# Kernel tuning notes

Hardware: AMD Instinct MI355X
Metric: run time of the kernel (lower is better)

## Reference

```python
import jax, jax.numpy as jnp
import numpy as np

EPS = 4.0 / 30.0  # epsilon / epoch from source
P_KEEP = 0.95     # random-response probability of keeping a column


def setup_inputs() -> dict:
    key = jax.random.key(0)
    ks = jax.random.split(key, 10)
    B, F, H, C = 262144, 160, 128, 10
    x1 = jax.random.normal(ks[0], (B, F), dtype=jnp.float32)
    x2 = jax.random.normal(ks[1], (B, F), dtype=jnp.float32)
    W1 = jax.random.normal(ks[2], (F, H), dtype=jnp.float32) * 0.05
    b1 = jax.random.normal(ks[3], (H,), dtype=jnp.float32) * 0.05
    W2 = jax.random.normal(ks[4], (F, H), dtype=jnp.float32) * 0.05
    b2 = jax.random.normal(ks[5], (H,), dtype=jnp.float32) * 0.05
    Ws = jax.random.normal(ks[6], (H, C), dtype=jnp.float32) * 0.05
    bs = jax.random.normal(ks[7], (C,), dtype=jnp.float32) * 0.05
    # standard Laplace(0,1) noise; scaled by sensitivity/eps inside reference
    noise_std = jax.random.laplace(ks[8], (B, H), dtype=jnp.float32)
    rr_uniform = jax.random.uniform(ks[9], (H,), dtype=jnp.float32)
    return {"x1": x1, "x2": x2, "W1": W1, "b1": b1, "W2": W2, "b2": b2,
            "Ws": Ws, "bs": bs, "noise_std": noise_std, "rr_uniform": rr_uniform}


def reference(x1, x2, W1, b1, W2, b2, Ws, bs, noise_std, rr_uniform):
    # client 1: linear -> DP noise -> random-response mask
    out1 = x1 @ W1 + b1                              # [B, 128]
    one_norm = jnp.sum(jnp.abs(out1), axis=1)        # per-row L1 norm
    sensitivity = jnp.max(one_norm) - jnp.min(one_norm)
    sensitivity = jax.lax.stop_gradient(sensitivity)  # .item() in torch: non-diff
    noise_mul = sensitivity / EPS
    out1 = out1 + noise_std * noise_mul              # Laplace(0, noise_mul) sample
    rr_mask = (rr_uniform < P_KEEP).astype(out1.dtype)  # [128] 0/1 mask
    out1 = out1 * rr_mask
    # client 2: plain linear
    out2 = x2 @ W2 + b2                              # [B, 128]
    # server: element-wise min then linear head
    server_input = jnp.minimum(out1, out2)
    return server_input @ Ws + bs                    # [B, 10]
```

## Files before the change

### kernel.cpp

```cpp
#include <hip/hip_runtime.h>
#include <hip/hip_bf16.h>
#include <float.h>


typedef __bf16 bf16x8 __attribute__((ext_vector_type(8)));
typedef __bf16 bf16x4 __attribute__((ext_vector_type(4)));
typedef float  f32x4  __attribute__((ext_vector_type(4)));

#define FDIM 160
#define HDIM 128
#define SROW 132

#define GL2LDS(g, l) __builtin_amdgcn_global_load_lds( \
    (const __attribute__((address_space(1))) unsigned int*)(g), \
    (__attribute__((address_space(3))) unsigned int*)(l), 16, 0, 0)

__global__ void k0_prep(const float* __restrict__ W1, const float* __restrict__ W2,
                        unsigned int* __restrict__ mmx,
                        __bf16* __restrict__ w1t, __bf16* __restrict__ w2t) {
    int tid = blockIdx.x * 256 + threadIdx.x;
    if (tid == 0) { mmx[0] = 0x7F7FFFFFu;  mmx[1] = 0u; }
    for (int idx = tid; idx < FDIM * HDIM; idx += gridDim.x * 256) {
        int k = idx >> 7, n = idx & 127;
        w1t[n * FDIM + k] = (__bf16)W1[idx];
        w2t[n * FDIM + k] = (__bf16)W2[idx];
    }
}

__device__ __forceinline__ bf16x8 pack8(f32x4 lo, f32x4 hi) {
    bf16x8 a;
    a[0] = (__bf16)lo[0]; a[1] = (__bf16)lo[1]; a[2] = (__bf16)lo[2]; a[3] = (__bf16)lo[3];
    a[4] = (__bf16)hi[0]; a[5] = (__bf16)hi[1]; a[6] = (__bf16)hi[2]; a[7] = (__bf16)hi[3];
    return a;
}

__global__ __launch_bounds__(256, 4) void k1_sens(
    const float* __restrict__ x1, const float* __restrict__ b1,
    const __bf16* __restrict__ w1t, unsigned int* __restrict__ mmx, int B)
{
    __shared__ __align__(16) char stg[2][10 * 1024];
    __shared__ float nbuf[2][4][16];

    const int lane = threadIdx.x & 63;
    const int wv   = threadIdx.x >> 6;
    const int m    = lane & 15;
    const int q    = lane >> 4;

    bf16x8 wf[2][5];
    f32x4  bv[2];
    #pragma unroll
    for (int cc = 0; cc < 2; ++cc) {
        const int ct = 2 * wv + cc;
        bv[cc] = *(const f32x4*)&b1[ct * 16 + q * 4];
        #pragma unroll
        for (int ks = 0; ks < 5; ++ks)
            wf[cc][ks] = *(const bf16x8*)(w1t + (ct * 16 + m) * FDIM + ks * 32 + q * 8);
    }

    const int nslab = B >> 4;
    auto stage = [&](int buf, int slab) {
        const float* rowp = x1 + (size_t)((slab << 4) + m) * FDIM + q * 8;
        for (int c = wv; c < 10; c += 4)
            GL2LDS(rowp + (c >> 1) * 32 + (c & 1) * 4, &stg[buf][c * 1024]);
    };

    float wmin = FLT_MAX, wmax = 0.0f;
    int it = blockIdx.x, cur = 0, iter = 0;
    stage(0, it);
    for (; it < nslab; it += gridDim.x) {
        asm volatile("s_waitcnt vmcnt(0)" ::: "memory");
        __syncthreads();
        if (iter > 0 && wv == 0 && lane < 16) {
            const int pb = (iter - 1) & 1;
            float nrm = nbuf[pb][0][m] + nbuf[pb][1][m] + nbuf[pb][2][m] + nbuf[pb][3][m];
            wmin = fminf(wmin, nrm); wmax = fmaxf(wmax, nrm);
        }
        if (it + (int)gridDim.x < nslab) stage(cur ^ 1, it + gridDim.x);

        f32x4 acc[2] = { bv[0], bv[1] };
        #pragma unroll
        for (int ks = 0; ks < 5; ++ks) {
            f32x4 lo = *(const f32x4*)&stg[cur][(2 * ks) * 1024 + lane * 16];
            f32x4 hi = *(const f32x4*)&stg[cur][(2 * ks + 1) * 1024 + lane * 16];
            bf16x8 a = pack8(lo, hi);
            acc[0] = __builtin_amdgcn_mfma_f32_16x16x32_bf16(wf[0][ks], a, acc[0], 0, 0, 0);
            acc[1] = __builtin_amdgcn_mfma_f32_16x16x32_bf16(wf[1][ks], a, acc[1], 0, 0, 0);
        }
        float part = 0.0f;
        #pragma unroll
        for (int cc = 0; cc < 2; ++cc)
            #pragma unroll
            for (int reg = 0; reg < 4; ++reg) part += fabsf(acc[cc][reg]);
        part += __shfl_xor(part, 16, 64);
        part += __shfl_xor(part, 32, 64);
        if (lane < 16) nbuf[iter & 1][wv][m] = part;
        cur ^= 1; ++iter;
    }
    __syncthreads();
    if (iter > 0 && wv == 0 && lane < 16) {
        const int pb = (iter - 1) & 1;
        float nrm = nbuf[pb][0][m] + nbuf[pb][1][m] + nbuf[pb][2][m] + nbuf[pb][3][m];
        wmin = fminf(wmin, nrm); wmax = fmaxf(wmax, nrm);
    }
    if (wv == 0) {
        #pragma unroll
        for (int off = 1; off < 16; off <<= 1) {
            wmin = fminf(wmin, __shfl_xor(wmin, off, 64));
            wmax = fmaxf(wmax, __shfl_xor(wmax, off, 64));
        }
        if (lane == 0) {
            atomicMin(&mmx[0], __float_as_uint(wmin));
            atomicMax(&mmx[1], __float_as_uint(wmax));
        }
    }
}

__global__ __launch_bounds__(256, 2) void k2_main(
    const float* __restrict__ x1, const float* __restrict__ x2,
    const float* __restrict__ b1, const float* __restrict__ b2,
    const float* __restrict__ Ws, const float* __restrict__ bs,
    const float* __restrict__ noise, const float* __restrict__ rru,
    const __bf16* __restrict__ w1t, const __bf16* __restrict__ w2t,
    const unsigned int* __restrict__ mmx, float* __restrict__ out, int B)
{
    __shared__ __align__(16) char   stg[2][28 * 1024];
    __shared__ __align__(16) __bf16 sbuf[16 * SROW];
    __shared__ __align__(16) float  obuf[160];

    const int lane = threadIdx.x & 63;
    const int wv   = threadIdx.x >> 6;
    const int m    = lane & 15;
    const int q    = lane >> 4;

    const float noise_mul = (__uint_as_float(mmx[1]) - __uint_as_float(mmx[0])) * 7.5f;

    bf16x8 wf1[2][5], wf2[2][5];
    f32x4  bv1[2], bv2[2];
    unsigned rmask = 0;
    #pragma unroll
    for (int cc = 0; cc < 2; ++cc) {
        const int ct = 2 * wv + cc;
        bv1[cc] = *(const f32x4*)&b1[ct * 16 + q * 4];
        bv2[cc] = *(const f32x4*)&b2[ct * 16 + q * 4];
        f32x4 r4 = *(const f32x4*)&rru[ct * 16 + q * 4];
        #pragma unroll
        for (int reg = 0; reg < 4; ++reg)
            if (r4[reg] < 0.95f) rmask |= 1u << (cc * 4 + reg);
        #pragma unroll
        for (int ks = 0; ks < 5; ++ks) {
            wf1[cc][ks] = *(const bf16x8*)(w1t + (ct * 16 + m) * FDIM + ks * 32 + q * 8);
            wf2[cc][ks] = *(const bf16x8*)(w2t + (ct * 16 + m) * FDIM + ks * 32 + q * 8);
        }
    }
    bf16x8 wsf[4];
    #pragma unroll
    for (int ks2 = 0; ks2 < 4; ++ks2)
        #pragma unroll
        for (int j = 0; j < 8; ++j) {
            int h = ks2 * 32 + q * 8 + j;
            wsf[ks2][j] = (__bf16)((m < 10) ? Ws[h * 10 + m] : 0.0f);
        }
    const float bsv = (m < 10) ? bs[m] : 0.0f;

    const int nslab = B >> 4;
    auto stage = [&](int buf, int slab) {
        const int r0 = slab << 4;
        const float* x1p = x1 + (size_t)(r0 + m) * FDIM + q * 8;
        const float* x2p = x2 + (size_t)(r0 + m) * FDIM + q * 8;
        const float* nzp = noise + (size_t)(r0 + m) * HDIM + q * 4;
        #pragma unroll
        for (int j = 0; j < 7; ++j) {
            const int c = wv * 7 + j;
            const float* g;
            if (c < 10)      g = x1p + (c >> 1) * 32 + (c & 1) * 4;
            else if (c < 20) g = x2p + ((c - 10) >> 1) * 32 + ((c - 10) & 1) * 4;
            else             g = nzp + (c - 20) * 16;
            GL2LDS(g, &stg[buf][c * 1024]);
        }
    };

    int it = blockIdx.x, cur = 0;
    stage(0, it);
    for (; it < nslab; it += gridDim.x) {
        asm volatile("s_waitcnt vmcnt(0)" ::: "memory");
        __syncthreads();
        if (it + (int)gridDim.x < nslab) stage(cur ^ 1, it + gridDim.x);

        f32x4 acc1[2] = { bv1[0], bv1[1] }, acc2[2] = { bv2[0], bv2[1] };
        #pragma unroll
        for (int ks = 0; ks < 5; ++ks) {
            f32x4 lo1 = *(const f32x4*)&stg[cur][(2 * ks) * 1024 + lane * 16];
            f32x4 hi1 = *(const f32x4*)&stg[cur][(2 * ks + 1) * 1024 + lane * 16];
            f32x4 lo2 = *(const f32x4*)&stg[cur][(10 + 2 * ks) * 1024 + lane * 16];
            f32x4 hi2 = *(const f32x4*)&stg[cur][(11 + 2 * ks) * 1024 + lane * 16];
            bf16x8 a1 = pack8(lo1, hi1), a2 = pack8(lo2, hi2);
            acc1[0] = __builtin_amdgcn_mfma_f32_16x16x32_bf16(wf1[0][ks], a1, acc1[0], 0, 0, 0);
            acc1[1] = __builtin_amdgcn_mfma_f32_16x16x32_bf16(wf1[1][ks], a1, acc1[1], 0, 0, 0);
            acc2[0] = __builtin_amdgcn_mfma_f32_16x16x32_bf16(wf2[0][ks], a2, acc2[0], 0, 0, 0);
            acc2[1] = __builtin_amdgcn_mfma_f32_16x16x32_bf16(wf2[1][ks], a2, acc2[1], 0, 0, 0);
        }
        #pragma unroll
        for (int cc = 0; cc < 2; ++cc) {
            f32x4 nz = *(const f32x4*)&stg[cur][(20 + 2 * wv + cc) * 1024 + lane * 16];
            bf16x4 pk;
            #pragma unroll
            for (int reg = 0; reg < 4; ++reg) {
                float v1 = acc1[cc][reg] + nz[reg] * noise_mul;
                v1 = ((rmask >> (cc * 4 + reg)) & 1u) ? v1 : 0.0f;
                pk[reg] = (__bf16)fminf(v1, acc2[cc][reg]);
            }
            *(bf16x4*)&sbuf[m * SROW + (2 * wv + cc) * 16 + q * 4] = pk;
        }
        __syncthreads();
        if (wv == 0) {
            f32x4 d = { bsv, bsv, bsv, bsv };
            #pragma unroll
            for (int ks2 = 0; ks2 < 4; ++ks2) {
                bf16x8 sf = *(const bf16x8*)&sbuf[m * SROW + ks2 * 32 + q * 8];
                d = __builtin_amdgcn_mfma_f32_16x16x32_bf16(sf, wsf[ks2], d, 0, 0, 0);
            }
            if (m < 10) {
                #pragma unroll
                for (int reg = 0; reg < 4; ++reg)
                    obuf[(q * 4 + reg) * 10 + m] = d[reg];
            }
            asm volatile("s_waitcnt lgkmcnt(0)" ::: "memory");
            if (lane < 40) {
                f32x4 o = *(const f32x4*)&obuf[lane * 4];
                *(f32x4*)(out + (size_t)it * 160 + lane * 4) = o;
            }
        }
        cur ^= 1;
    }
}

extern "C" void kernel_launch(void* const* d_in, const int* in_sizes, int n_in,
                              void* d_out, int out_size, void* d_ws, size_t ws_size,
                              hipStream_t stream) {
    const float* x1    = (const float*)d_in[0];
    const float* x2    = (const float*)d_in[1];
    const float* W1    = (const float*)d_in[2];
    const float* b1    = (const float*)d_in[3];
    const float* W2    = (const float*)d_in[4];
    const float* b2    = (const float*)d_in[5];
    const float* Ws    = (const float*)d_in[6];
    const float* bs    = (const float*)d_in[7];
    const float* noise = (const float*)d_in[8];
    const float* rru   = (const float*)d_in[9];
    float* out = (float*)d_out;
    const int B = in_sizes[0] / FDIM;

    unsigned int* mmx = (unsigned int*)d_ws;
    __bf16* w1t = (__bf16*)((char*)d_ws + 256);
    __bf16* w2t = (__bf16*)((char*)d_ws + 256 + 40960);

    hipLaunchKernelGGL(k0_prep, dim3(64), dim3(256), 0, stream, W1, W2, mmx, w1t, w2t);
    hipLaunchKernelGGL(k1_sens, dim3(1024), dim3(256), 0, stream, x1, b1, w1t, mmx, B);
    hipLaunchKernelGGL(k2_main, dim3(512), dim3(256), 0, stream,
                       x1, x2, b1, b2, Ws, bs, noise, rru, w1t, w2t, mmx, out, B);
}
```

Before: 481.2 us.

## Triple-buffer staging with partial vmcnt waits and register-prefetched noise

Both kernels move from double-buffered LDS staging with full vmcnt(0) waits to a three-stage ring with prefetch distance two, waiting only on the oldest batch through partial vmcnt counts and raw s_barrier. In the main kernel the noise tile no longer goes through LDS; it is loaded straight into registers one iteration ahead. The output head is now computed redundantly by every wave, and each wave writes one quarter of the rows directly to global memory, which removes the obuf round-trip. The aim is to keep more loads in flight and reduce barrier stalls. The cost is more LDS per block, hand-counted vmcnt values that must match the real number of outstanding loads, and redundant loads of slab 0 when a prefetch runs past the end.

```diff
diff --git a/kernel.cpp b/kernel.cpp
--- a/kernel.cpp
+++ b/kernel.cpp
@@ -38,7 +38,7 @@
     const float* __restrict__ x1, const float* __restrict__ b1,
     const __bf16* __restrict__ w1t, unsigned int* __restrict__ mmx, int B)
 {
-    __shared__ __align__(16) char stg[2][10 * 1024];
+    __shared__ __align__(16) char stg[3][10 * 1024];
     __shared__ float nbuf[2][4][16];
 
     const int lane = threadIdx.x & 63;
@@ -58,43 +58,60 @@
     }
 
     const int nslab = B >> 4;
+    const int G = gridDim.x;
+
     auto stage = [&](int buf, int slab) {
+        if (slab >= nslab) slab = 0;
         const float* rowp = x1 + (size_t)((slab << 4) + m) * FDIM + q * 8;
-        for (int c = wv; c < 10; c += 4)
-            GL2LDS(rowp + (c >> 1) * 32 + (c & 1) * 4, &stg[buf][c * 1024]);
+        if (wv < 2) {
+            #pragma unroll
+            for (int j = 0; j < 3; ++j) {
+                const int c = wv * 3 + j;
+                GL2LDS(rowp + (c >> 1) * 32 + (c & 1) * 4, &stg[buf][c * 1024]);
+            }
+        } else {
+            #pragma unroll
+            for (int j = 0; j < 2; ++j) {
+                const int c = 6 + (wv - 2) * 2 + j;
+                GL2LDS(rowp + (c >> 1) * 32 + (c & 1) * 4, &stg[buf][c * 1024]);
+            }
+        }
     };
 
     float wmin = FLT_MAX, wmax = 0.0f;
-    int it = blockIdx.x, cur = 0, iter = 0;
-    stage(0, it);
-    for (; it < nslab; it += gridDim.x) {
-        asm volatile("s_waitcnt vmcnt(0)" ::: "memory");
-        __syncthreads();
-        if (iter > 0 && wv == 0 && lane < 16) {
-            const int pb = (iter - 1) & 1;
-            float nrm = nbuf[pb][0][m] + nbuf[pb][1][m] + nbuf[pb][2][m] + nbuf[pb][3][m];
-            wmin = fminf(wmin, nrm); wmax = fmaxf(wmax, nrm);
-        }
-        if (it + (int)gridDim.x < nslab) stage(cur ^ 1, it + gridDim.x);
-
-        f32x4 acc[2] = { bv[0], bv[1] };
-        #pragma unroll
-        for (int ks = 0; ks < 5; ++ks) {
-            f32x4 lo = *(const f32x4*)&stg[cur][(2 * ks) * 1024 + lane * 16];
-            f32x4 hi = *(const f32x4*)&stg[cur][(2 * ks + 1) * 1024 + lane * 16];
-            bf16x8 a = pack8(lo, hi);
-            acc[0] = __builtin_amdgcn_mfma_f32_16x16x32_bf16(wf[0][ks], a, acc[0], 0, 0, 0);
-            acc[1] = __builtin_amdgcn_mfma_f32_16x16x32_bf16(wf[1][ks], a, acc[1], 0, 0, 0);
-        }
-        float part = 0.0f;
-        #pragma unroll
-        for (int cc = 0; cc < 2; ++cc)
-            #pragma unroll
-            for (int reg = 0; reg < 4; ++reg) part += fabsf(acc[cc][reg]);
-        part += __shfl_xor(part, 16, 64);
-        part += __shfl_xor(part, 32, 64);
-        if (lane < 16) nbuf[iter & 1][wv][m] = part;
-        cur ^= 1; ++iter;
+    int it = blockIdx.x, iter = 0, cur = 0;
+    if (it < nslab) {
+        stage(0, it);
+        stage(1, it + G);
+        for (; it < nslab; it += G) {
+            if (wv < 2) asm volatile("s_waitcnt vmcnt(3) lgkmcnt(0)\n\ts_barrier" ::: "memory");
+            else        asm volatile("s_waitcnt vmcnt(2) lgkmcnt(0)\n\ts_barrier" ::: "memory");
+            if (iter > 0 && wv == 0 && lane < 16) {
+                const int pb = (iter - 1) & 1;
+                float nrm = nbuf[pb][0][m] + nbuf[pb][1][m] + nbuf[pb][2][m] + nbuf[pb][3][m];
+                wmin = fminf(wmin, nrm); wmax = fmaxf(wmax, nrm);
+            }
+            f32x4 acc[2] = { bv[0], bv[1] };
+            #pragma unroll
+            for (int ks = 0; ks < 5; ++ks) {
+                f32x4 lo = *(const f32x4*)&stg[cur][(2 * ks) * 1024 + lane * 16];
+                f32x4 hi = *(const f32x4*)&stg[cur][(2 * ks + 1) * 1024 + lane * 16];
+                bf16x8 a = pack8(lo, hi);
+                acc[0] = __builtin_amdgcn_mfma_f32_16x16x32_bf16(wf[0][ks], a, acc[0], 0, 0, 0);
+                acc[1] = __builtin_amdgcn_mfma_f32_16x16x32_bf16(wf[1][ks], a, acc[1], 0, 0, 0);
+            }
+            float part = 0.0f;
+            #pragma unroll
+            for (int cc = 0; cc < 2; ++cc)
+                #pragma unroll
+                for (int reg = 0; reg < 4; ++reg) part += fabsf(acc[cc][reg]);
+            part += __shfl_xor(part, 16, 64);
+            part += __shfl_xor(part, 32, 64);
+            if (lane < 16) nbuf[iter & 1][wv][m] = part;
+            { int nb = cur + 2; if (nb >= 3) nb -= 3; stage(nb, it + 2 * G); }
+            cur = (cur == 2) ? 0 : cur + 1;
+            ++iter;
+        }
     }
     __syncthreads();
     if (iter > 0 && wv == 0 && lane < 16) {
@@ -123,9 +140,8 @@
     const __bf16* __restrict__ w1t, const __bf16* __restrict__ w2t,
     const unsigned int* __restrict__ mmx, float* __restrict__ out, int B)
 {
-    __shared__ __align__(16) char   stg[2][28 * 1024];
+    __shared__ __align__(16) char   stg[3][20 * 1024];
     __shared__ __align__(16) __bf16 sbuf[16 * SROW];
-    __shared__ __align__(16) float  obuf[160];
 
     const int lane = threadIdx.x & 63;
     const int wv   = threadIdx.x >> 6;
@@ -163,75 +179,90 @@
     const float bsv = (m < 10) ? bs[m] : 0.0f;
 
     const int nslab = B >> 4;
+    const int G = gridDim.x;
+
     auto stage = [&](int buf, int slab) {
+        if (slab >= nslab) slab = 0;
         const int r0 = slab << 4;
         const float* x1p = x1 + (size_t)(r0 + m) * FDIM + q * 8;
         const float* x2p = x2 + (size_t)(r0 + m) * FDIM + q * 8;
-        const float* nzp = noise + (size_t)(r0 + m) * HDIM + q * 4;
-        #pragma unroll
-        for (int j = 0; j < 7; ++j) {
-            const int c = wv * 7 + j;
-            const float* g;
-            if (c < 10)      g = x1p + (c >> 1) * 32 + (c & 1) * 4;
-            else if (c < 20) g = x2p + ((c - 10) >> 1) * 32 + ((c - 10) & 1) * 4;
-            else             g = nzp + (c - 20) * 16;
+        #pragma unroll
+        for (int j = 0; j < 5; ++j) {
+            const int c = wv * 5 + j;
+            const float* g = (c < 10) ? (x1p + (c >> 1) * 32 + (c & 1) * 4)
+                                      : (x2p + ((c - 10) >> 1) * 32 + ((c - 10) & 1) * 4);
             GL2LDS(g, &stg[buf][c * 1024]);
         }
     };
 
+#define K2_BODY(VMWS)                                                              \
+  {                                                                                \
+    asm volatile("s_waitcnt vmcnt(" VMWS ") lgkmcnt(0)\n\ts_barrier" ::: "memory");\
+          \
+    int nsl_ = it + G; if (nsl_ >= nslab) nsl_ = 0;                                \
+    const float* nzp_ = noise + (size_t)((nsl_ << 4) + m) * HDIM + q * 4;          \
+    f32x4 nz_nxt0 = *(const f32x4*)(nzp_ + (2 * wv) * 16);                         \
+    f32x4 nz_nxt1 = *(const f32x4*)(nzp_ + (2 * wv + 1) * 16);                     \
+    f32x4 acc1[2] = { bv1[0], bv1[1] }, acc2[2] = { bv2[0], bv2[1] };              \
+    _Pragma("unroll")                                                              \
+    for (int ks = 0; ks < 5; ++ks) {                                               \
+        f32x4 lo1 = *(const f32x4*)&stg[cur][(2 * ks) * 1024 + lane * 16];         \
+        f32x4 hi1 = *(const f32x4*)&stg[cur][(2 * ks + 1) * 1024 + lane * 16];     \
+        f32x4 lo2 = *(const f32x4*)&stg[cur][(10 + 2 * ks) * 1024 + lane * 16];    \
+        f32x4 hi2 = *(const f32x4*)&stg[cur][(11 + 2 * ks) * 1024 + lane * 16];    \
+        bf16x8 a1 = pack8(lo1, hi1), a2 = pack8(lo2, hi2);                         \
+        acc1[0] = __builtin_amdgcn_mfma_f32_16x16x32_bf16(wf1[0][ks], a1, acc1[0], 0, 0, 0); \
+        acc1[1] = __builtin_amdgcn_mfma_f32_16x16x32_bf16(wf1[1][ks], a1, acc1[1], 0, 0, 0); \
+        acc2[0] = __builtin_amdgcn_mfma_f32_16x16x32_bf16(wf2[0][ks], a2, acc2[0], 0, 0, 0); \
+        acc2[1] = __builtin_amdgcn_mfma_f32_16x16x32_bf16(wf2[1][ks], a2, acc2[1], 0, 0, 0); \
+    }                                                                              \
+    _Pragma("unroll")                                                              \
+    for (int cc = 0; cc < 2; ++cc) {                                               \
+        bf16x4 pk;                                                                 \
+        _Pragma("unroll")                                                          \
+        for (int reg = 0; reg < 4; ++reg) {                                        \
+            float v1 = acc1[cc][reg] + ((cc == 0) ? nz_cur0[reg] : nz_cur1[reg]) * noise_mul; \
+            v1 = ((rmask >> (cc * 4 + reg)) & 1u) ? v1 : 0.0f;                     \
+            pk[reg] = (__bf16)fminf(v1, acc2[cc][reg]);                            \
+        }                                                                          \
+        *(bf16x4*)&sbuf[m * SROW + (2 * wv + cc) * 16 + q * 4] = pk;               \
+    }                                                                              \
+    asm volatile("s_waitcnt lgkmcnt(0)\n\ts_barrier" ::: "memory");                \
+      \
+      \
+    f32x4 d = { bsv, bsv, bsv, bsv };                                              \
+    _Pragma("unroll")                                                              \
+    for (int ks2 = 0; ks2 < 4; ++ks2) {                                            \
+        bf16x8 sf = *(const bf16x8*)&sbuf[m * SROW + ks2 * 32 + q * 8];            \
+        d = __builtin_amdgcn_mfma_f32_16x16x32_bf16(sf, wsf[ks2], d, 0, 0, 0);     \
+    }                                                                              \
+    if (q == wv && m < 10) {                                                       \
+        _Pragma("unroll")                                                          \
+        for (int reg = 0; reg < 4; ++reg)                                          \
+            out[(size_t)(it * 16 + q * 4 + reg) * 10 + m] = d[reg];                \
+    }                                                                              \
+    { int nb_ = cur + 2; if (nb_ >= 3) nb_ -= 3; stage(nb_, it + 2 * G); }         \
+    nz_cur0 = nz_nxt0; nz_cur1 = nz_nxt1;                                          \
+  }
+
     int it = blockIdx.x, cur = 0;
-    stage(0, it);
-    for (; it < nslab; it += gridDim.x) {
-        asm volatile("s_waitcnt vmcnt(0)" ::: "memory");
-        __syncthreads();
-        if (it + (int)gridDim.x < nslab) stage(cur ^ 1, it + gridDim.x);
-
-        f32x4 acc1[2] = { bv1[0], bv1[1] }, acc2[2] = { bv2[0], bv2[1] };
-        #pragma unroll
-        for (int ks = 0; ks < 5; ++ks) {
-            f32x4 lo1 = *(const f32x4*)&stg[cur][(2 * ks) * 1024 + lane * 16];
-            f32x4 hi1 = *(const f32x4*)&stg[cur][(2 * ks + 1) * 1024 + lane * 16];
-            f32x4 lo2 = *(const f32x4*)&stg[cur][(10 + 2 * ks) * 1024 + lane * 16];
-            f32x4 hi2 = *(const f32x4*)&stg[cur][(11 + 2 * ks) * 1024 + lane * 16];
-            bf16x8 a1 = pack8(lo1, hi1), a2 = pack8(lo2, hi2);
-            acc1[0] = __builtin_amdgcn_mfma_f32_16x16x32_bf16(wf1[0][ks], a1, acc1[0], 0, 0, 0);
-            acc1[1] = __builtin_amdgcn_mfma_f32_16x16x32_bf16(wf1[1][ks], a1, acc1[1], 0, 0, 0);
-            acc2[0] = __builtin_amdgcn_mfma_f32_16x16x32_bf16(wf2[0][ks], a2, acc2[0], 0, 0, 0);
-            acc2[1] = __builtin_amdgcn_mfma_f32_16x16x32_bf16(wf2[1][ks], a2, acc2[1], 0, 0, 0);
-        }
-        #pragma unroll
-        for (int cc = 0; cc < 2; ++cc) {
-            f32x4 nz = *(const f32x4*)&stg[cur][(20 + 2 * wv + cc) * 1024 + lane * 16];
-            bf16x4 pk;
-            #pragma unroll
-            for (int reg = 0; reg < 4; ++reg) {
-                float v1 = acc1[cc][reg] + nz[reg] * noise_mul;
-                v1 = ((rmask >> (cc * 4 + reg)) & 1u) ? v1 : 0.0f;
-                pk[reg] = (__bf16)fminf(v1, acc2[cc][reg]);
-            }
-            *(bf16x4*)&sbuf[m * SROW + (2 * wv + cc) * 16 + q * 4] = pk;
-        }
-        __syncthreads();
-        if (wv == 0) {
-            f32x4 d = { bsv, bsv, bsv, bsv };
-            #pragma unroll
-            for (int ks2 = 0; ks2 < 4; ++ks2) {
-                bf16x8 sf = *(const bf16x8*)&sbuf[m * SROW + ks2 * 32 + q * 8];
-                d = __builtin_amdgcn_mfma_f32_16x16x32_bf16(sf, wsf[ks2], d, 0, 0, 0);
-            }
-            if (m < 10) {
-                #pragma unroll
-                for (int reg = 0; reg < 4; ++reg)
-                    obuf[(q * 4 + reg) * 10 + m] = d[reg];
-            }
-            asm volatile("s_waitcnt lgkmcnt(0)" ::: "memory");
-            if (lane < 40) {
-                f32x4 o = *(const f32x4*)&obuf[lane * 4];
-                *(f32x4*)(out + (size_t)it * 160 + lane * 4) = o;
-            }
-        }
-        cur ^= 1;
-    }
+    if (it < nslab) {
+        f32x4 nz_cur0, nz_cur1;
+        {
+            const float* nzp0 = noise + (size_t)((it << 4) + m) * HDIM + q * 4;
+            nz_cur0 = *(const f32x4*)(nzp0 + (2 * wv) * 16);
+            nz_cur1 = *(const f32x4*)(nzp0 + (2 * wv + 1) * 16);
+        }
+        stage(0, it);
+        stage(1, it + G);
+        K2_BODY("5");
+        it += G; cur = 1;
+        for (; it < nslab; it += G) {
+            K2_BODY("11");
+            cur = (cur == 2) ? 0 : cur + 1;
+        }
+    }
+#undef K2_BODY
 }
 
 extern "C" void kernel_launch(void* const* d_in, const int* in_sizes, int n_in,
```

Result: faster. 470.5 us (-2.2%).

## Deepen prefetch pipelines, load noise to registers, defer head GEMM a step

Applied to the files above, without the earlier changes.

The sensitivity kernel switches to a triple-buffered LDS ring with two slabs in flight and partial vmcnt waits, so it no longer drains all loads every iteration. The main kernel loads noise straight into registers instead of staging it in LDS, which shrinks the LDS footprint enough to raise occupancy to 3 blocks and a 768-block grid. It double-buffers the server-input tile and runs the head GEMM one iteration late, dropping the second __syncthreads. Output is written directly from MFMA registers, split across waves, instead of through an LDS bounce buffer. The cost is hand-counted vmcnt waits and out-of-range slab clamping, which are fragile and add redundant tail loads.

```diff
diff --git a/kernel.cpp b/kernel.cpp
--- a/kernel.cpp
+++ b/kernel.cpp
@@ -38,7 +38,7 @@
     const float* __restrict__ x1, const float* __restrict__ b1,
     const __bf16* __restrict__ w1t, unsigned int* __restrict__ mmx, int B)
 {
-    __shared__ __align__(16) char stg[2][10 * 1024];
+    __shared__ __align__(16) char stg[3][10 * 1024];
     __shared__ float nbuf[2][4][16];
 
     const int lane = threadIdx.x & 63;
@@ -58,43 +58,60 @@
     }
 
     const int nslab = B >> 4;
+    const int G = gridDim.x;
+
     auto stage = [&](int buf, int slab) {
+        if (slab >= nslab) slab = 0;
         const float* rowp = x1 + (size_t)((slab << 4) + m) * FDIM + q * 8;
-        for (int c = wv; c < 10; c += 4)
-            GL2LDS(rowp + (c >> 1) * 32 + (c & 1) * 4, &stg[buf][c * 1024]);
+        if (wv < 2) {
+            #pragma unroll
+            for (int j = 0; j < 3; ++j) {
+                const int c = wv * 3 + j;
+                GL2LDS(rowp + (c >> 1) * 32 + (c & 1) * 4, &stg[buf][c * 1024]);
+            }
+        } else {
+            #pragma unroll
+            for (int j = 0; j < 2; ++j) {
+                const int c = 6 + (wv - 2) * 2 + j;
+                GL2LDS(rowp + (c >> 1) * 32 + (c & 1) * 4, &stg[buf][c * 1024]);
+            }
+        }
     };
 
     float wmin = FLT_MAX, wmax = 0.0f;
-    int it = blockIdx.x, cur = 0, iter = 0;
-    stage(0, it);
-    for (; it < nslab; it += gridDim.x) {
-        asm volatile("s_waitcnt vmcnt(0)" ::: "memory");
-        __syncthreads();
-        if (iter > 0 && wv == 0 && lane < 16) {
-            const int pb = (iter - 1) & 1;
-            float nrm = nbuf[pb][0][m] + nbuf[pb][1][m] + nbuf[pb][2][m] + nbuf[pb][3][m];
-            wmin = fminf(wmin, nrm); wmax = fmaxf(wmax, nrm);
-        }
-        if (it + (int)gridDim.x < nslab) stage(cur ^ 1, it + gridDim.x);
-
-        f32x4 acc[2] = { bv[0], bv[1] };
-        #pragma unroll
-        for (int ks = 0; ks < 5; ++ks) {
-            f32x4 lo = *(const f32x4*)&stg[cur][(2 * ks) * 1024 + lane * 16];
-            f32x4 hi = *(const f32x4*)&stg[cur][(2 * ks + 1) * 1024 + lane * 16];
-            bf16x8 a = pack8(lo, hi);
-            acc[0] = __builtin_amdgcn_mfma_f32_16x16x32_bf16(wf[0][ks], a, acc[0], 0, 0, 0);
-            acc[1] = __builtin_amdgcn_mfma_f32_16x16x32_bf16(wf[1][ks], a, acc[1], 0, 0, 0);
-        }
-        float part = 0.0f;
-        #pragma unroll
-        for (int cc = 0; cc < 2; ++cc)
-            #pragma unroll
-            for (int reg = 0; reg < 4; ++reg) part += fabsf(acc[cc][reg]);
-        part += __shfl_xor(part, 16, 64);
-        part += __shfl_xor(part, 32, 64);
-        if (lane < 16) nbuf[iter & 1][wv][m] = part;
-        cur ^= 1; ++iter;
+    int it = blockIdx.x, iter = 0, cur = 0;
+    if (it < nslab) {
+        stage(0, it);
+        stage(1, it + G);
+        for (; it < nslab; it += G) {
+            if (wv < 2) asm volatile("s_waitcnt vmcnt(3) lgkmcnt(0)\n\ts_barrier" ::: "memory");
+            else        asm volatile("s_waitcnt vmcnt(2) lgkmcnt(0)\n\ts_barrier" ::: "memory");
+            if (iter > 0 && wv == 0 && lane < 16) {
+                const int pb = (iter - 1) & 1;
+                float nrm = nbuf[pb][0][m] + nbuf[pb][1][m] + nbuf[pb][2][m] + nbuf[pb][3][m];
+                wmin = fminf(wmin, nrm); wmax = fmaxf(wmax, nrm);
+            }
+            f32x4 acc[2] = { bv[0], bv[1] };
+            #pragma unroll
+            for (int ks = 0; ks < 5; ++ks) {
+                f32x4 lo = *(const f32x4*)&stg[cur][(2 * ks) * 1024 + lane * 16];
+                f32x4 hi = *(const f32x4*)&stg[cur][(2 * ks + 1) * 1024 + lane * 16];
+                bf16x8 a = pack8(lo, hi);
+                acc[0] = __builtin_amdgcn_mfma_f32_16x16x32_bf16(wf[0][ks], a, acc[0], 0, 0, 0);
+                acc[1] = __builtin_amdgcn_mfma_f32_16x16x32_bf16(wf[1][ks], a, acc[1], 0, 0, 0);
+            }
+            float part = 0.0f;
+            #pragma unroll
+            for (int cc = 0; cc < 2; ++cc)
+                #pragma unroll
+                for (int reg = 0; reg < 4; ++reg) part += fabsf(acc[cc][reg]);
+            part += __shfl_xor(part, 16, 64);
+            part += __shfl_xor(part, 32, 64);
+            if (lane < 16) nbuf[iter & 1][wv][m] = part;
+            { int nb = cur + 2; if (nb >= 3) nb -= 3; stage(nb, it + 2 * G); }
+            cur = (cur == 2) ? 0 : cur + 1;
+            ++iter;
+        }
     }
     __syncthreads();
     if (iter > 0 && wv == 0 && lane < 16) {
@@ -113,9 +130,10 @@
             atomicMax(&mmx[1], __float_as_uint(wmax));
         }
     }
-}
-
-__global__ __launch_bounds__(256, 2) void k2_main(
+    asm volatile("s_waitcnt vmcnt(0)" ::: "memory");
+}
+
+__global__ __launch_bounds__(256, 3) void k2_main(
     const float* __restrict__ x1, const float* __restrict__ x2,
     const float* __restrict__ b1, const float* __restrict__ b2,
     const float* __restrict__ Ws, const float* __restrict__ bs,
@@ -123,9 +141,8 @@
     const __bf16* __restrict__ w1t, const __bf16* __restrict__ w2t,
     const unsigned int* __restrict__ mmx, float* __restrict__ out, int B)
 {
-    __shared__ __align__(16) char   stg[2][28 * 1024];
-    __shared__ __align__(16) __bf16 sbuf[16 * SROW];
-    __shared__ __align__(16) float  obuf[160];
+    __shared__ __align__(16) char   stg[2][20 * 1024];
+    __shared__ __align__(16) __bf16 sbuf[2][16 * SROW];
 
     const int lane = threadIdx.x & 63;
     const int wv   = threadIdx.x >> 6;
@@ -163,36 +180,38 @@
     const float bsv = (m < 10) ? bs[m] : 0.0f;
 
     const int nslab = B >> 4;
+    const int G = gridDim.x;
+
     auto stage = [&](int buf, int slab) {
+        if (slab >= nslab) slab = 0;
         const int r0 = slab << 4;
         const float* x1p = x1 + (size_t)(r0 + m) * FDIM + q * 8;
         const float* x2p = x2 + (size_t)(r0 + m) * FDIM + q * 8;
-        const float* nzp = noise + (size_t)(r0 + m) * HDIM + q * 4;
-        #pragma unroll
-        for (int j = 0; j < 7; ++j) {
-            const int c = wv * 7 + j;
-            const float* g;
-            if (c < 10)      g = x1p + (c >> 1) * 32 + (c & 1) * 4;
-            else if (c < 20) g = x2p + ((c - 10) >> 1) * 32 + ((c - 10) & 1) * 4;
-            else             g = nzp + (c - 20) * 16;
+        #pragma unroll
+        for (int j = 0; j < 5; ++j) {
+            const int c = wv * 5 + j;
+            const float* g = (c < 10) ? (x1p + (c >> 1) * 32 + (c & 1) * 4)
+                                      : (x2p + ((c - 10) >> 1) * 32 + ((c - 10) & 1) * 4);
             GL2LDS(g, &stg[buf][c * 1024]);
         }
     };
 
-    int it = blockIdx.x, cur = 0;
-    stage(0, it);
-    for (; it < nslab; it += gridDim.x) {
-        asm volatile("s_waitcnt vmcnt(0)" ::: "memory");
-        __syncthreads();
-        if (it + (int)gridDim.x < nslab) stage(cur ^ 1, it + gridDim.x);
-
+    f32x4 nzc0, nzc1, nzn0, nzn1;
+    auto loadnz = [&](int slab, f32x4& a, f32x4& b) {
+        if (slab >= nslab) slab = 0;
+        const float* nzp = noise + (size_t)((slab << 4) + m) * HDIM + q * 4;
+        a = *(const f32x4*)(nzp + (2 * wv) * 16);
+        b = *(const f32x4*)(nzp + (2 * wv + 1) * 16);
+    };
+
+    auto main_step = [&](int p) {
         f32x4 acc1[2] = { bv1[0], bv1[1] }, acc2[2] = { bv2[0], bv2[1] };
         #pragma unroll
         for (int ks = 0; ks < 5; ++ks) {
-            f32x4 lo1 = *(const f32x4*)&stg[cur][(2 * ks) * 1024 + lane * 16];
-            f32x4 hi1 = *(const f32x4*)&stg[cur][(2 * ks + 1) * 1024 + lane * 16];
-            f32x4 lo2 = *(const f32x4*)&stg[cur][(10 + 2 * ks) * 1024 + lane * 16];
-            f32x4 hi2 = *(const f32x4*)&stg[cur][(11 + 2 * ks) * 1024 + lane * 16];
+            f32x4 lo1 = *(const f32x4*)&stg[p][(2 * ks) * 1024 + lane * 16];
+            f32x4 hi1 = *(const f32x4*)&stg[p][(2 * ks + 1) * 1024 + lane * 16];
+            f32x4 lo2 = *(const f32x4*)&stg[p][(10 + 2 * ks) * 1024 + lane * 16];
+            f32x4 hi2 = *(const f32x4*)&stg[p][(11 + 2 * ks) * 1024 + lane * 16];
             bf16x8 a1 = pack8(lo1, hi1), a2 = pack8(lo2, hi2);
             acc1[0] = __builtin_amdgcn_mfma_f32_16x16x32_bf16(wf1[0][ks], a1, acc1[0], 0, 0, 0);
             acc1[1] = __builtin_amdgcn_mfma_f32_16x16x32_bf16(wf1[1][ks], a1, acc1[1], 0, 0, 0);
@@ -201,37 +220,64 @@
         }
         #pragma unroll
         for (int cc = 0; cc < 2; ++cc) {
-            f32x4 nz = *(const f32x4*)&stg[cur][(20 + 2 * wv + cc) * 1024 + lane * 16];
             bf16x4 pk;
             #pragma unroll
             for (int reg = 0; reg < 4; ++reg) {
-                float v1 = acc1[cc][reg] + nz[reg] * noise_mul;
+                float v1 = acc1[cc][reg] + ((cc == 0) ? nzc0[reg] : nzc1[reg]) * noise_mul;
                 v1 = ((rmask >> (cc * 4 + reg)) & 1u) ? v1 : 0.0f;
                 pk[reg] = (__bf16)fminf(v1, acc2[cc][reg]);
             }
-            *(bf16x4*)&sbuf[m * SROW + (2 * wv + cc) * 16 + q * 4] = pk;
-        }
-        __syncthreads();
-        if (wv == 0) {
-            f32x4 d = { bsv, bsv, bsv, bsv };
-            #pragma unroll
-            for (int ks2 = 0; ks2 < 4; ++ks2) {
-                bf16x8 sf = *(const bf16x8*)&sbuf[m * SROW + ks2 * 32 + q * 8];
-                d = __builtin_amdgcn_mfma_f32_16x16x32_bf16(sf, wsf[ks2], d, 0, 0, 0);
-            }
-            if (m < 10) {
-                #pragma unroll
-                for (int reg = 0; reg < 4; ++reg)
-                    obuf[(q * 4 + reg) * 10 + m] = d[reg];
-            }
-            asm volatile("s_waitcnt lgkmcnt(0)" ::: "memory");
-            if (lane < 40) {
-                f32x4 o = *(const f32x4*)&obuf[lane * 4];
-                *(f32x4*)(out + (size_t)it * 160 + lane * 4) = o;
-            }
-        }
-        cur ^= 1;
-    }
+            *(bf16x4*)&sbuf[p][m * SROW + (2 * wv + cc) * 16 + q * 4] = pk;
+        }
+    };
+
+    auto head = [&](int hp, int slab) {
+        f32x4 d = { bsv, bsv, bsv, bsv };
+        #pragma unroll
+        for (int ks2 = 0; ks2 < 4; ++ks2) {
+            bf16x8 sf = *(const bf16x8*)&sbuf[hp][m * SROW + ks2 * 32 + q * 8];
+            d = __builtin_amdgcn_mfma_f32_16x16x32_bf16(sf, wsf[ks2], d, 0, 0, 0);
+        }
+        if (q == wv && m < 10) {
+            #pragma unroll
+            for (int reg = 0; reg < 4; ++reg)
+                out[(size_t)(slab * 16 + q * 4 + reg) * 10 + m] = d[reg];
+        }
+    };
+
+    int it = blockIdx.x;
+    int pit = it;
+    loadnz(it, nzc0, nzc1);
+    stage(0, it);
+    asm volatile("s_waitcnt vmcnt(0) lgkmcnt(0)\n\ts_barrier" ::: "memory");
+    stage(1, it + G);
+    __builtin_amdgcn_sched_barrier(0);
+    loadnz(it + G, nzn0, nzn1);
+    main_step(0);
+    nzc0 = nzn0; nzc1 = nzn1;
+    it += G;
+    asm volatile("s_waitcnt vmcnt(2) lgkmcnt(0)\n\ts_barrier" ::: "memory");
+    stage(0, it + G);
+    __builtin_amdgcn_sched_barrier(0);
+    loadnz(it + G, nzn0, nzn1);
+    main_step(1);
+    head(0, pit);
+    nzc0 = nzn0; nzc1 = nzn1;
+    pit = it; it += G;
+    int p = 0;
+    for (; it < nslab; it += G) {
+        asm volatile("s_waitcnt vmcnt(6) lgkmcnt(0)\n\ts_barrier" ::: "memory");
+        stage(p ^ 1, it + G);
+        __builtin_amdgcn_sched_barrier(0);
+        loadnz(it + G, nzn0, nzn1);
+        main_step(p);
+        head(p ^ 1, pit);
+        nzc0 = nzn0; nzc1 = nzn1;
+        pit = it; p ^= 1;
+    }
+    asm volatile("s_waitcnt lgkmcnt(0)\n\ts_barrier" ::: "memory");
+    head(p ^ 1, pit);
+    asm volatile("s_waitcnt vmcnt(0)" ::: "memory");
 }
 
 extern "C" void kernel_launch(void* const* d_in, const int* in_sizes, int n_in,
@@ -256,6 +302,6 @@
 
     hipLaunchKernelGGL(k0_prep, dim3(64), dim3(256), 0, stream, W1, W2, mmx, w1t, w2t);
     hipLaunchKernelGGL(k1_sens, dim3(1024), dim3(256), 0, stream, x1, b1, w1t, mmx, B);
-    hipLaunchKernelGGL(k2_main, dim3(512), dim3(256), 0, stream,
+    hipLaunchKernelGGL(k2_main, dim3(768), dim3(256), 0, stream,
                        x1, x2, b1, b2, Ws, bs, noise, rru, w1t, w2t, mmx, out, B);
 }
```

Measured after the change: 558.5 us. 1.16x slower.
